# Performance work log

Hardware: AMD Instinct MI355X
Metric: run time of the kernel (lower is better)

Reference implementation:

```python
import jax, jax.numpy as jnp
import numpy as np

BITS = 108

def setup_inputs() -> dict:
    key = jax.random.key(0)
    kA, kB = jax.random.split(key)
    shape = (262144, BITS)
    A = jax.random.randint(kA, shape, 0, 2).astype(jnp.float32)
    B = jax.random.randint(kB, shape, 0, 2).astype(jnp.float32)
    return {"A": A, "B": B}

def reference(A, B):
    # Soft-logic gates on {0,1} floats: XOR=a+b-2ab, AND=ab, OR=a+b-ab.
    P = A + B - 2.0 * A * B          # propagate, [batch, 108]
    G = A * B                        # generate,  [batch, 108]
    # Ripple-carry: c_{i+1} = OR(g_i, AND(p_i, c_i)); scan over bit axis.
    Pm = jnp.moveaxis(P, -1, 0)      # [108, batch]
    Gm = jnp.moveaxis(G, -1, 0)
    c0 = jnp.zeros(A.shape[:-1], dtype=A.dtype)

    def step(c, pg):
        p, g = pg
        pc = p * c
        c_next = g + pc - g * pc     # OR(g, p*c)
        return c_next, c             # emit carry-IN of this bit

    c_last, carries = jax.lax.scan(step, c0, (Pm, Gm))
    all_carries = jnp.moveaxis(carries, 0, -1)        # [batch, 108]
    S = P + all_carries - 2.0 * P * all_carries        # XOR(P, carries)
    Cout = c_last[..., None]                           # [batch, 1]
    return (S, Cout)
```

## Files before the change

### kernel.cpp

```cpp
#include <hip/hip_runtime.h>

#define BITS 108
#define F4PR 27
#define ACT  54

typedef float f32x4 __attribute__((ext_vector_type(4)));

__global__ __launch_bounds__(256) void rca108_kernel(
    const f32x4* __restrict__ A4, const f32x4* __restrict__ B4,
    f32x4* __restrict__ S4, float* __restrict__ C)
{
    const int gtid = blockIdx.x * blockDim.x + threadIdx.x;
    const int wid  = gtid >> 6;
    const int l    = threadIdx.x & 63;
    const int pos  = (l < F4PR) ? l : l - F4PR;
    const int li   = (l < ACT) ? l : (ACT - 1);
    const size_t g = (size_t)wid * ACT + li;

    const f32x4 av = A4[g];
    const f32x4 bv = B4[g];
    const unsigned an = (unsigned)(av.x > 0.5f)
                      | ((unsigned)(av.y > 0.5f) << 1)
                      | ((unsigned)(av.z > 0.5f) << 2)
                      | ((unsigned)(av.w > 0.5f) << 3);
    const unsigned bn = (unsigned)(bv.x > 0.5f)
                      | ((unsigned)(bv.y > 0.5f) << 1)
                      | ((unsigned)(bv.z > 0.5f) << 2)
                      | ((unsigned)(bv.w > 0.5f) << 3);
    const unsigned sum = an + bn;
    const unsigned Gn  = sum >> 4;
    const unsigned Pn  = ((sum & 0xFu) == 0xFu) ? 1u : 0u;

    const unsigned v    = Gn | (Pn << 1);
    const unsigned prev = __shfl_up(v, 1);
    unsigned x = (pos == 0) ? (0u | (1u << 1) | (1u << 2)) : prev;

    #pragma unroll
    for (int d = 1; d <= 16; d <<= 1) {
        const unsigned y = __shfl_up(x, d);
        const bool take = (l >= d) && ((x & 4u) == 0u);
        const unsigned Ghi = x & 1u, Phi = (x >> 1) & 1u;
        const unsigned Glo = y & 1u, Plo = (y >> 1) & 1u;
        const unsigned comb = (Ghi | (Phi & Glo))
                            | ((Phi & Plo) << 1)
                            | ((x | y) & 4u);
        x = take ? comb : x;
    }
    const unsigned cin = x & 1u;
    const unsigned s   = sum + cin;

    f32x4 out;
    out.x = (float)( s       & 1u);
    out.y = (float)((s >> 1) & 1u);
    out.z = (float)((s >> 2) & 1u);
    out.w = (float)((s >> 3) & 1u);
    if (l < ACT) {
        __builtin_nontemporal_store(out, &S4[g]);
        if (pos == F4PR - 1) {
            const int row = wid * 2 + (l >= F4PR);
            __builtin_nontemporal_store((float)(s >> 4), &C[row]);
        }
    }
}

extern "C" void kernel_launch(void* const* d_in, const int* in_sizes, int n_in,
                              void* d_out, int out_size, void* d_ws, size_t ws_size,
                              hipStream_t stream) {
    const f32x4* A4 = (const f32x4*)d_in[0];
    const f32x4* B4 = (const f32x4*)d_in[1];
    float* S = (float*)d_out;
    const int nrows = in_sizes[0] / BITS;
    float* C = S + (size_t)nrows * BITS;

    const int nwaves = nrows / 2;
    const int threads = nwaves * 64;
    const int block = 256;
    const int grid = threads / block;
    rca108_kernel<<<grid, block, 0, stream>>>(A4, B4, (f32x4*)S, C);
}
```

Before: 51.89 us.

## Replace shuffle carry scan with ballot add-carry trick and grid-stride loop

Result: slower. 55.22 us (+6.4%).

```diff
diff --git a/kernel.cpp b/kernel.cpp
--- a/kernel.cpp
+++ b/kernel.cpp
@@ -3,62 +3,57 @@
 #define BITS 108
 #define F4PR 27
 #define ACT  54
+#define NPAIRS 131072
+#define NBLK 2048
+#define TPB  256
 
 typedef float f32x4 __attribute__((ext_vector_type(4)));
 
-__global__ __launch_bounds__(256) void rca108_kernel(
+__global__ __launch_bounds__(TPB) void rca108_kernel(
     const f32x4* __restrict__ A4, const f32x4* __restrict__ B4,
     f32x4* __restrict__ S4, float* __restrict__ C)
 {
-    const int gtid = blockIdx.x * blockDim.x + threadIdx.x;
-    const int wid  = gtid >> 6;
-    const int l    = threadIdx.x & 63;
-    const int pos  = (l < F4PR) ? l : l - F4PR;
-    const int li   = (l < ACT) ? l : (ACT - 1);
-    const size_t g = (size_t)wid * ACT + li;
+    const int l     = threadIdx.x & 63;
+    const int half  = (l >= F4PR) ? 1 : 0;
+    const int pos   = l - half * F4PR;
+    const int lidx  = (l < ACT) ? l : (ACT - 1);
+    const int wid0  = (blockIdx.x * TPB + threadIdx.x) >> 6;
+    const int nwav  = (NBLK * TPB) >> 6;
 
-    const f32x4 av = A4[g];
-    const f32x4 bv = B4[g];
-    const unsigned an = (unsigned)(av.x > 0.5f)
-                      | ((unsigned)(av.y > 0.5f) << 1)
-                      | ((unsigned)(av.z > 0.5f) << 2)
-                      | ((unsigned)(av.w > 0.5f) << 3);
-    const unsigned bn = (unsigned)(bv.x > 0.5f)
-                      | ((unsigned)(bv.y > 0.5f) << 1)
-                      | ((unsigned)(bv.z > 0.5f) << 2)
-                      | ((unsigned)(bv.w > 0.5f) << 3);
-    const unsigned sum = an + bn;
-    const unsigned Gn  = sum >> 4;
-    const unsigned Pn  = ((sum & 0xFu) == 0xFu) ? 1u : 0u;
+    #pragma unroll 2
+    for (int w = wid0; w < NPAIRS; w += nwav) {
+        const size_t g = (size_t)w * ACT + lidx;
+        const f32x4 av = A4[g];
+        const f32x4 bv = B4[g];
+        const unsigned an = (unsigned)(av.x > 0.5f)
+                          | ((unsigned)(av.y > 0.5f) << 1)
+                          | ((unsigned)(av.z > 0.5f) << 2)
+                          | ((unsigned)(av.w > 0.5f) << 3);
+        const unsigned bn = (unsigned)(bv.x > 0.5f)
+                          | ((unsigned)(bv.y > 0.5f) << 1)
+                          | ((unsigned)(bv.z > 0.5f) << 2)
+                          | ((unsigned)(bv.w > 0.5f) << 3);
+        const unsigned sum = an + bn;
 
-    const unsigned v    = Gn | (Pn << 1);
-    const unsigned prev = __shfl_up(v, 1);
-    unsigned x = (pos == 0) ? (0u | (1u << 1) | (1u << 2)) : prev;
+        const unsigned long long gm = __ballot(sum >= 16u);
+        const unsigned long long pm = __ballot(sum == 15u);
 
-    #pragma unroll
-    for (int d = 1; d <= 16; d <<= 1) {
-        const unsigned y = __shfl_up(x, d);
-        const bool take = (l >= d) && ((x & 4u) == 0u);
-        const unsigned Ghi = x & 1u, Phi = (x >> 1) & 1u;
-        const unsigned Glo = y & 1u, Plo = (y >> 1) & 1u;
-        const unsigned comb = (Ghi | (Phi & Glo))
-                            | ((Phi & Plo) << 1)
-                            | ((x | y) & 4u);
-        x = take ? comb : x;
-    }
-    const unsigned cin = x & 1u;
-    const unsigned s   = sum + cin;
+        const unsigned rg = (unsigned)(gm >> (half * F4PR)) & 0x7FFFFFFu;
+        const unsigned rp = (unsigned)(pm >> (half * F4PR)) & 0x7FFFFFFu;
+        const unsigned q  = rg | rp;
+        const unsigned k  = (q + rg) ^ q ^ rg;
+        const unsigned cin = (k >> pos) & 1u;
+        const unsigned s   = sum + cin;
 
-    f32x4 out;
-    out.x = (float)( s       & 1u);
-    out.y = (float)((s >> 1) & 1u);
-    out.z = (float)((s >> 2) & 1u);
-    out.w = (float)((s >> 3) & 1u);
-    if (l < ACT) {
-        __builtin_nontemporal_store(out, &S4[g]);
-        if (pos == F4PR - 1) {
-            const int row = wid * 2 + (l >= F4PR);
-            __builtin_nontemporal_store((float)(s >> 4), &C[row]);
+        f32x4 out;
+        out.x = (float)( s       & 1u);
+        out.y = (float)((s >> 1) & 1u);
+        out.z = (float)((s >> 2) & 1u);
+        out.w = (float)((s >> 3) & 1u);
+        if (l < ACT) {
+            __builtin_nontemporal_store(out, &S4[g]);
+            if (pos == F4PR - 1)
+                __builtin_nontemporal_store((float)(s >> 4), &C[2 * w + half]);
         }
     }
 }
@@ -71,10 +66,7 @@
     float* S = (float*)d_out;
     const int nrows = in_sizes[0] / BITS;
     float* C = S + (size_t)nrows * BITS;
+    (void)nrows;
 
-    const int nwaves = nrows / 2;
-    const int threads = nwaves * 64;
-    const int block = 256;
-    const int grid = threads / block;
-    rca108_kernel<<<grid, block, 0, stream>>>(A4, B4, (f32x4*)S, C);
+    rca108_kernel<<<NBLK, TPB, 0, stream>>>(A4, B4, (f32x4*)S, C);
 }
```
